# Optimization experiments

Measured on AMD Instinct MI355X. Metric: run time of the kernel, lower is better.

## Reference

```python
import jax, jax.numpy as jnp
import numpy as np

D_MODEL = 1024
N_HEADS = 16
HEAD_DIM = D_MODEL // N_HEADS  # 64


def setup_inputs() -> dict:
    key = jax.random.key(0)
    ks = jax.random.split(key, 6)
    scale_in = 1.0 / np.sqrt(D_MODEL)
    scale_hd = 1.0 / np.sqrt(N_HEADS * HEAD_DIM)
    inputs_q = jax.random.normal(ks[0], (4, 2048, D_MODEL), dtype=jnp.float32)
    # DenseGeneral kernels: [d_model, n_heads, head_dim] for q/k/v, [n_heads, head_dim, d_model] for out.
    Wq = jax.random.normal(ks[1], (D_MODEL, N_HEADS, HEAD_DIM), dtype=jnp.float32) * scale_in
    Wk = jax.random.normal(ks[2], (D_MODEL, N_HEADS, HEAD_DIM), dtype=jnp.float32) * scale_in
    Wv = jax.random.normal(ks[3], (D_MODEL, N_HEADS, HEAD_DIM), dtype=jnp.float32) * scale_in
    Wo = jax.random.normal(ks[4], (N_HEADS, HEAD_DIM, D_MODEL), dtype=jnp.float32) * scale_hd
    bq = jnp.zeros((N_HEADS, HEAD_DIM), dtype=jnp.float32)
    bk = jnp.zeros((N_HEADS, HEAD_DIM), dtype=jnp.float32)
    bv = jnp.zeros((N_HEADS, HEAD_DIM), dtype=jnp.float32)
    bo = jnp.zeros((D_MODEL,), dtype=jnp.float32)
    return {"inputs_q": inputs_q, "Wq": Wq, "bq": bq, "Wk": Wk, "bk": bk,
            "Wv": Wv, "bv": bv, "Wo": Wo, "bo": bo}


def reference(inputs_q, Wq, bq, Wk, bk, Wv, bv, Wo, bo):
    # Self-attention: inputs_kv = inputs_q.
    # QKV projections (DenseGeneral axis=-1 -> (heads, head_dim)).
    q = jnp.einsum('bsf,fhd->bshd', inputs_q, Wq) + bq  # [B,S,H,D]
    k = jnp.einsum('bsf,fhd->bshd', inputs_q, Wk) + bk
    v = jnp.einsum('bsf,fhd->bshd', inputs_q, Wv) + bv
    # Scaled dot-product attention (naive: full [B,H,S,S] scores, as in source).
    q = q / jnp.sqrt(jnp.asarray(HEAD_DIM, dtype=q.dtype))
    scores = jnp.einsum('bqhd,bkhd->bhqk', q, k)  # [B,H,Sq,Sk]
    attn = jax.nn.softmax(scores, axis=-1)
    x = jnp.einsum('bhqk,bkhd->bqhd', attn, v)  # [B,S,H,D]
    # Output projection over (heads, head_dim).
    out = jnp.einsum('bqhd,hdf->bqf', x, Wo) + bo  # [B,S,d_model]
    return out
```

## Files before the change

kernel.cpp:

```cpp
#include <hip/hip_runtime.h>
#include <math.h>

typedef __bf16 bf16;
typedef __attribute__((ext_vector_type(4))) __bf16 bf16x4;
typedef __attribute__((ext_vector_type(8))) __bf16 bf16x8;
typedef __attribute__((ext_vector_type(4))) float f32x4;

#define LOG2E 1.44269504088896340736f

__device__ __forceinline__ f32x4 mfma16(bf16x8 a, bf16x8 b, f32x4 c) {
  return __builtin_amdgcn_mfma_f32_16x16x32_bf16(a, b, c, 0, 0, 0);
}

__device__ __forceinline__ void load_lds16(const bf16* g, bf16* l) {
  __builtin_amdgcn_global_load_lds(
      (__attribute__((address_space(1))) void*)(g),
      (__attribute__((address_space(3))) void*)(l), 16, 0, 0);
}

__global__ __launch_bounds__(256) void cvt_x(const float* __restrict__ x,
                                             bf16* __restrict__ xb) {
  int i = (blockIdx.x * 256 + threadIdx.x) * 8;
  float4 a = *(const float4*)&x[i];
  float4 b = *(const float4*)&x[i + 4];
  bf16x8 v;
  v[0] = (bf16)a.x; v[1] = (bf16)a.y; v[2] = (bf16)a.z; v[3] = (bf16)a.w;
  v[4] = (bf16)b.x; v[5] = (bf16)b.y; v[6] = (bf16)b.z; v[7] = (bf16)b.w;
  *(bf16x8*)&xb[i] = v;
}

__global__ __launch_bounds__(256) void wtrans(
    const float* __restrict__ Wq, const float* __restrict__ Wk,
    const float* __restrict__ Wv, const float* __restrict__ Wo,
    bf16* __restrict__ Wcat, bf16* __restrict__ WoT, float qscale) {
  __shared__ float t[32][33];
  const int z = blockIdx.z;
  const float* src = (z == 0) ? Wq : (z == 1) ? Wk : (z == 2) ? Wv : Wo;
  bf16* dst = (z == 3) ? WoT : (Wcat + (size_t)z * 1024 * 1024);
  const float scale = (z == 0) ? qscale : 1.0f;
  int c0 = blockIdx.x * 32, r0 = blockIdx.y * 32;
  for (int i = threadIdx.y; i < 32; i += 8)
    t[i][threadIdx.x] = src[(r0 + i) * 1024 + c0 + threadIdx.x];
  __syncthreads();
  for (int i = threadIdx.y; i < 32; i += 8)
    dst[(c0 + i) * 1024 + r0 + threadIdx.x] = (bf16)(t[threadIdx.x][i] * scale);
}

__global__ __launch_bounds__(256) void vtrans(const bf16* __restrict__ Vs,
                                              bf16* __restrict__ Vt) {
  __shared__ bf16 t[64][72];
  const int bh = blockIdx.y;
  const int s0 = blockIdx.x * 64;
  const size_t base = (size_t)bh * 2048 * 64;
  const int tid = threadIdx.x;
  {
    int r = tid >> 3, c = (tid & 7) * 8;
    *(uint4*)&t[r][c]      = *(const uint4*)&Vs[base + (size_t)(s0 + r) * 64 + c];
    *(uint4*)&t[r + 32][c] = *(const uint4*)&Vs[base + (size_t)(s0 + r + 32) * 64 + c];
  }
  __syncthreads();
  int d = tid >> 2, sc = (tid & 3) * 16;
  bf16 tmp[16];
#pragma unroll
  for (int k = 0; k < 16; k++) tmp[k] = t[sc + k][d];
  *(uint4*)&Vt[base + (size_t)d * 2048 + s0 + sc]     = *(uint4*)&tmp[0];
  *(uint4*)&Vt[base + (size_t)d * 2048 + s0 + sc + 8] = *(uint4*)&tmp[8];
}

template <int MODE>
__global__ __launch_bounds__(256, 2) void gemm_bt(
    const bf16* __restrict__ A, const bf16* __restrict__ Bt, int N, int K,
    bf16* __restrict__ Qo, bf16* __restrict__ Ko, bf16* __restrict__ Vo,
    const float* __restrict__ b0, const float* __restrict__ b1,
    const float* __restrict__ b2,
    float* __restrict__ Co, const float* __restrict__ bias) {
  __shared__ bf16 lA[128 * 32];
  __shared__ bf16 lB[128 * 32];
  const int tid = threadIdx.x;
  const int lane = tid & 63, w = tid >> 6;
  const int l16 = lane & 15, quad = lane >> 4;
  const int swz = (l16 >> 2) & 3;
  const int wm = w >> 1, wn = w & 1;
  const int id = blockIdx.x;
  const int xcd = id & 7, local = id >> 3;
  const int m0 = (xcd * 8 + (local & 7)) * 128;
  const int n0 = (local >> 3) * 128;

  const int srow = w * 16 + (lane >> 2);
  const int scol = (((lane & 3) ^ ((lane >> 4) & 3)) * 8);
  const bf16* Ag = A + (size_t)(m0 + srow) * K + scol;
  const bf16* Bg = Bt + (size_t)(n0 + srow) * K + scol;
  bf16* lAw = &lA[w * 16 * 32];
  bf16* lBw = &lB[w * 16 * 32];

  f32x4 acc[4][4] = {};
  for (int k0 = 0; k0 < K; k0 += 32) {
    __syncthreads();
    load_lds16(Ag + k0, lAw);
    load_lds16(Ag + k0 + (size_t)64 * K, lAw + 64 * 32);
    load_lds16(Bg + k0, lBw);
    load_lds16(Bg + k0 + (size_t)64 * K, lBw + 64 * 32);
    __syncthreads();
    bf16x8 af[4], bfr[4];
#pragma unroll
    for (int i = 0; i < 4; i++)
      af[i] = *(const bf16x8*)&lA[(wm * 64 + i * 16 + l16) * 32 + (quad ^ swz) * 8];
#pragma unroll
    for (int i = 0; i < 4; i++)
      bfr[i] = *(const bf16x8*)&lB[(wn * 64 + i * 16 + l16) * 32 + (quad ^ swz) * 8];
#pragma unroll
    for (int i = 0; i < 4; i++)
#pragma unroll
      for (int j = 0; j < 4; j++)
        acc[i][j] = mfma16(af[i], bfr[j], acc[i][j]);
  }

  if (MODE == 0) {
    const int which = n0 >> 10;
    bf16* dst = (which == 0) ? Qo : (which == 1) ? Ko : Vo;
    const float* bsrc = (which == 0) ? b0 : (which == 1) ? b1 : b2;
    const float bscale = (which == 0) ? (0.125f * LOG2E) : 1.0f;
#pragma unroll
    for (int j = 0; j < 4; j++) {
      const int nn = (n0 & 1023) + wn * 64 + j * 16 + l16;
      const int h = nn >> 6, d = nn & 63;
      const float bias_v = bsrc[nn] * bscale;
#pragma unroll
      for (int i = 0; i < 4; i++) {
#pragma unroll
        for (int rg = 0; rg < 4; rg++) {
          const int grow = m0 + wm * 64 + i * 16 + quad * 4 + rg;
          const int bb = grow >> 11, s = grow & 2047;
          dst[((size_t)(bb * 16 + h) * 2048 + s) * 64 + d] =
              (bf16)(acc[i][j][rg] + bias_v);
        }
      }
    }
  } else {
#pragma unroll
    for (int j = 0; j < 4; j++) {
      const int gcol = n0 + wn * 64 + j * 16 + l16;
      const float bias_v = bias[gcol];
#pragma unroll
      for (int i = 0; i < 4; i++) {
#pragma unroll
        for (int rg = 0; rg < 4; rg++) {
          const int grow = m0 + wm * 64 + i * 16 + quad * 4 + rg;
          Co[(size_t)grow * N + gcol] = acc[i][j][rg] + bias_v;
        }
      }
    }
  }
}

__global__ __launch_bounds__(256, 2) void attn(const bf16* __restrict__ Q,
                                               const bf16* __restrict__ Kb,
                                               const bf16* __restrict__ Vt,
                                               bf16* __restrict__ X2) {
  __shared__ bf16 lK[2][2][64][32];
  __shared__ bf16 lV[2][2][64][32];
  __shared__ bf16 lP[4][64][72];
  const int tid = threadIdx.x;
  const int lane = tid & 63, w = tid >> 6;
  const int l16 = lane & 15, quad = lane >> 4;
  const int swz = (l16 >> 2) & 3;
  const int bh = blockIdx.x & 63;
  const int q0 = (blockIdx.x >> 6) * 256;
  const int bb = bh >> 4, h = bh & 15;
  const size_t base = (size_t)bh * 2048 * 64;

  bf16x8 aq[4][2];
#pragma unroll
  for (int mi = 0; mi < 4; mi++)
#pragma unroll
    for (int kh = 0; kh < 2; kh++)
      aq[mi][kh] = *(const bf16x8*)&Q[base + (size_t)(q0 + w * 64 + mi * 16 + l16) * 64 + kh * 32 + quad * 8];

  f32x4 o_acc[4][4] = {};
  float l_r[4] = {0.f, 0.f, 0.f, 0.f};

  const int drow = lane >> 2;
  const int dcol = (((lane & 3) ^ ((lane >> 4) & 3)) * 8);
  const bf16* Kg = Kb + base + (size_t)(w * 16 + drow) * 64 + dcol;
  const bf16* Vg = Vt + base + (size_t)(w * 16 + drow) * 2048 + dcol;

  load_lds16(Kg, &lK[0][0][w * 16][0]);
  load_lds16(Kg + 32, &lK[0][1][w * 16][0]);
  load_lds16(Vg, &lV[0][0][w * 16][0]);
  load_lds16(Vg + 32, &lV[0][1][w * 16][0]);

  for (int kt = 0; kt < 32; kt++) {
    const int p = kt & 1;
    __syncthreads();
    if (kt + 1 < 32) {
      const bf16* kg = Kg + (size_t)(kt + 1) * 64 * 64;
      const bf16* vg = Vg + (kt + 1) * 64;
      load_lds16(kg, &lK[p ^ 1][0][w * 16][0]);
      load_lds16(kg + 32, &lK[p ^ 1][1][w * 16][0]);
      load_lds16(vg, &lV[p ^ 1][0][w * 16][0]);
      load_lds16(vg + 32, &lV[p ^ 1][1][w * 16][0]);
    }

#pragma unroll
    for (int g = 0; g < 2; g++) {
      f32x4 s[2][4] = {};
#pragma unroll
      for (int n2 = 0; n2 < 2; n2++) {
        const int ni = g * 2 + n2;
        bf16x8 ak0 = *(const bf16x8*)&lK[p][0][ni * 16 + l16][(quad ^ swz) * 8];
        bf16x8 ak1 = *(const bf16x8*)&lK[p][1][ni * 16 + l16][(quad ^ swz) * 8];
#pragma unroll
        for (int mi = 0; mi < 4; mi++) {
          s[n2][mi] = mfma16(ak0, aq[mi][0], s[n2][mi]);
          s[n2][mi] = mfma16(ak1, aq[mi][1], s[n2][mi]);
        }
      }
#pragma unroll
      for (int n2 = 0; n2 < 2; n2++) {
        const int ni = g * 2 + n2;
#pragma unroll
        for (int mi = 0; mi < 4; mi++) {
          bf16x4 pw;
          float lp = 0.f;
#pragma unroll
          for (int rg = 0; rg < 4; rg++) {
            float pv = __builtin_amdgcn_exp2f(s[n2][mi][rg]);
            lp += pv;
            pw[rg] = (bf16)pv;
          }
          l_r[mi] += lp;
          *(bf16x4*)&lP[w][mi * 16 + l16][ni * 16 + quad * 4] = pw;
        }
      }
    }

    bf16x8 vf0[4], vf1[4];
#pragma unroll
    for (int di = 0; di < 4; di++) {
      vf0[di] = *(const bf16x8*)&lV[p][0][di * 16 + l16][(quad ^ swz) * 8];
      vf1[di] = *(const bf16x8*)&lV[p][1][di * 16 + l16][(quad ^ swz) * 8];
    }
#pragma unroll
    for (int mi = 0; mi < 4; mi++) {
      bf16x8 ap0 = *(const bf16x8*)&lP[w][mi * 16 + l16][quad * 8];
      bf16x8 ap1 = *(const bf16x8*)&lP[w][mi * 16 + l16][32 + quad * 8];
#pragma unroll
      for (int di = 0; di < 4; di++) {
        o_acc[mi][di] = mfma16(ap0, vf0[di], o_acc[mi][di]);
        o_acc[mi][di] = mfma16(ap1, vf1[di], o_acc[mi][di]);
      }
    }
  }

#pragma unroll
  for (int mi = 0; mi < 4; mi++) {
    float l = l_r[mi];
    l += __shfl_xor(l, 16);
    l += __shfl_xor(l, 32);
    l_r[mi] = 1.f / l;
  }
#pragma unroll
  for (int mi = 0; mi < 4; mi++)
#pragma unroll
    for (int rg = 0; rg < 4; rg++) {
      float inv = __shfl(l_r[mi], quad * 4 + rg);
      int s = q0 + w * 64 + mi * 16 + quad * 4 + rg;
#pragma unroll
      for (int di = 0; di < 4; di++) {
        float v = o_acc[mi][di][rg] * inv;
        X2[((size_t)bb * 2048 + s) * 1024 + h * 64 + di * 16 + l16] = (bf16)v;
      }
    }
}

extern "C" void kernel_launch(void* const* d_in, const int* in_sizes, int n_in,
                              void* d_out, int out_size, void* d_ws, size_t ws_size,
                              hipStream_t stream) {
  const float* x  = (const float*)d_in[0];
  const float* Wq = (const float*)d_in[1];
  const float* bq = (const float*)d_in[2];
  const float* Wk = (const float*)d_in[3];
  const float* bk = (const float*)d_in[4];
  const float* Wv = (const float*)d_in[5];
  const float* bv = (const float*)d_in[6];
  const float* Wo = (const float*)d_in[7];
  const float* bo = (const float*)d_in[8];
  float* out = (float*)d_out;

  char* ws = (char*)d_ws;
  bf16* Xb   = (bf16*)(ws);
  bf16* Wcat = (bf16*)(ws + 16777216);
  bf16* WoT  = (bf16*)(ws + 23068672);
  bf16* Qb   = (bf16*)(ws + 25165824);
  bf16* Kbf  = (bf16*)(ws + 41943040);
  bf16* Vt   = (bf16*)(ws + 58720256);
  bf16* Vs   = (bf16*)d_out;
  bf16* X2   = Xb;

  cvt_x<<<4096, 256, 0, stream>>>(x, Xb);
  wtrans<<<dim3(32, 32, 4), dim3(32, 8), 0, stream>>>(
      Wq, Wk, Wv, Wo, Wcat, WoT, 0.125f * LOG2E);

  gemm_bt<0><<<1536, 256, 0, stream>>>(Xb, Wcat, 3072, 1024,
      Qb, Kbf, Vs, bq, bk, bv, nullptr, nullptr);

  vtrans<<<dim3(32, 64), 256, 0, stream>>>(Vs, Vt);

  attn<<<512, 256, 0, stream>>>(Qb, Kbf, Vt, X2);

  gemm_bt<1><<<512, 256, 0, stream>>>(X2, WoT, 1024, 1024,
      nullptr, nullptr, nullptr, nullptr, nullptr, nullptr, out, bo);
}
```

Before: 276.2 us.

## Load K/V fragments directly from global memory in single-wave attention blocks

The attention kernel switches from 256-thread blocks that stage K and V tiles in double-buffered shared memory to 64-thread single-wave blocks that read K and V MFMA fragments straight from global memory, leaving only the P tile in LDS. This removes the block-wide barriers and LDS staging traffic and raises the number of blocks from 512 to 2048. In exchange each wave now fetches K/V itself without reuse across waves, so global/L2 traffic grows fourfold, and nothing prefetches ahead of use, so load latency has to be covered by occupancy instead.

```diff
diff --git a/kernel.cpp b/kernel.cpp
--- a/kernel.cpp
+++ b/kernel.cpp
@@ -153,19 +153,15 @@
   }
 }
 
-__global__ __launch_bounds__(256, 2) void attn(const bf16* __restrict__ Q,
-                                               const bf16* __restrict__ Kb,
-                                               const bf16* __restrict__ Vt,
-                                               bf16* __restrict__ X2) {
-  __shared__ bf16 lK[2][2][64][32];
-  __shared__ bf16 lV[2][2][64][32];
-  __shared__ bf16 lP[4][64][72];
-  const int tid = threadIdx.x;
-  const int lane = tid & 63, w = tid >> 6;
+__global__ __launch_bounds__(64, 3) void attn(const bf16* __restrict__ Q,
+                                              const bf16* __restrict__ Kb,
+                                              const bf16* __restrict__ Vt,
+                                              bf16* __restrict__ X2) {
+  __shared__ bf16 lP[64][72];
+  const int lane = threadIdx.x;
   const int l16 = lane & 15, quad = lane >> 4;
-  const int swz = (l16 >> 2) & 3;
   const int bh = blockIdx.x & 63;
-  const int q0 = (blockIdx.x >> 6) * 256;
+  const int q0 = (blockIdx.x >> 6) * 64;
   const int bb = bh >> 4, h = bh & 15;
   const size_t base = (size_t)bh * 2048 * 64;
 
@@ -174,41 +170,24 @@
   for (int mi = 0; mi < 4; mi++)
 #pragma unroll
     for (int kh = 0; kh < 2; kh++)
-      aq[mi][kh] = *(const bf16x8*)&Q[base + (size_t)(q0 + w * 64 + mi * 16 + l16) * 64 + kh * 32 + quad * 8];
+      aq[mi][kh] = *(const bf16x8*)&Q[base + (size_t)(q0 + mi * 16 + l16) * 64 + kh * 32 + quad * 8];
 
   f32x4 o_acc[4][4] = {};
   float l_r[4] = {0.f, 0.f, 0.f, 0.f};
 
-  const int drow = lane >> 2;
-  const int dcol = (((lane & 3) ^ ((lane >> 4) & 3)) * 8);
-  const bf16* Kg = Kb + base + (size_t)(w * 16 + drow) * 64 + dcol;
-  const bf16* Vg = Vt + base + (size_t)(w * 16 + drow) * 2048 + dcol;
-
-  load_lds16(Kg, &lK[0][0][w * 16][0]);
-  load_lds16(Kg + 32, &lK[0][1][w * 16][0]);
-  load_lds16(Vg, &lV[0][0][w * 16][0]);
-  load_lds16(Vg + 32, &lV[0][1][w * 16][0]);
+  const bf16* Kp = Kb + base + (size_t)l16 * 64 + quad * 8;
+  const bf16* Vp = Vt + base + (size_t)l16 * 2048 + quad * 8;
 
   for (int kt = 0; kt < 32; kt++) {
-    const int p = kt & 1;
-    __syncthreads();
-    if (kt + 1 < 32) {
-      const bf16* kg = Kg + (size_t)(kt + 1) * 64 * 64;
-      const bf16* vg = Vg + (kt + 1) * 64;
-      load_lds16(kg, &lK[p ^ 1][0][w * 16][0]);
-      load_lds16(kg + 32, &lK[p ^ 1][1][w * 16][0]);
-      load_lds16(vg, &lV[p ^ 1][0][w * 16][0]);
-      load_lds16(vg + 32, &lV[p ^ 1][1][w * 16][0]);
-    }
-
 #pragma unroll
     for (int g = 0; g < 2; g++) {
       f32x4 s[2][4] = {};
 #pragma unroll
       for (int n2 = 0; n2 < 2; n2++) {
         const int ni = g * 2 + n2;
-        bf16x8 ak0 = *(const bf16x8*)&lK[p][0][ni * 16 + l16][(quad ^ swz) * 8];
-        bf16x8 ak1 = *(const bf16x8*)&lK[p][1][ni * 16 + l16][(quad ^ swz) * 8];
+        const bf16* kr = Kp + (size_t)(kt * 64 + ni * 16) * 64;
+        bf16x8 ak0 = *(const bf16x8*)kr;
+        bf16x8 ak1 = *(const bf16x8*)(kr + 32);
 #pragma unroll
         for (int mi = 0; mi < 4; mi++) {
           s[n2][mi] = mfma16(ak0, aq[mi][0], s[n2][mi]);
@@ -229,7 +208,7 @@
             pw[rg] = (bf16)pv;
           }
           l_r[mi] += lp;
-          *(bf16x4*)&lP[w][mi * 16 + l16][ni * 16 + quad * 4] = pw;
+          *(bf16x4*)&lP[mi * 16 + l16][ni * 16 + quad * 4] = pw;
         }
       }
     }
@@ -237,13 +216,14 @@
     bf16x8 vf0[4], vf1[4];
 #pragma unroll
     for (int di = 0; di < 4; di++) {
-      vf0[di] = *(const bf16x8*)&lV[p][0][di * 16 + l16][(quad ^ swz) * 8];
-      vf1[di] = *(const bf16x8*)&lV[p][1][di * 16 + l16][(quad ^ swz) * 8];
+      const bf16* vr = Vp + (size_t)(di * 16) * 2048 + kt * 64;
+      vf0[di] = *(const bf16x8*)vr;
+      vf1[di] = *(const bf16x8*)(vr + 32);
     }
 #pragma unroll
     for (int mi = 0; mi < 4; mi++) {
-      bf16x8 ap0 = *(const bf16x8*)&lP[w][mi * 16 + l16][quad * 8];
-      bf16x8 ap1 = *(const bf16x8*)&lP[w][mi * 16 + l16][32 + quad * 8];
+      bf16x8 ap0 = *(const bf16x8*)&lP[mi * 16 + l16][quad * 8];
+      bf16x8 ap1 = *(const bf16x8*)&lP[mi * 16 + l16][32 + quad * 8];
 #pragma unroll
       for (int di = 0; di < 4; di++) {
         o_acc[mi][di] = mfma16(ap0, vf0[di], o_acc[mi][di]);
@@ -264,7 +244,7 @@
 #pragma unroll
     for (int rg = 0; rg < 4; rg++) {
       float inv = __shfl(l_r[mi], quad * 4 + rg);
-      int s = q0 + w * 64 + mi * 16 + quad * 4 + rg;
+      int s = q0 + mi * 16 + quad * 4 + rg;
 #pragma unroll
       for (int di = 0; di < 4; di++) {
         float v = o_acc[mi][di][rg] * inv;
@@ -306,7 +286,7 @@
 
   vtrans<<<dim3(32, 64), 256, 0, stream>>>(Vs, Vt);
 
-  attn<<<512, 256, 0, stream>>>(Qb, Kbf, Vt, X2);
+  attn<<<2048, 64, 0, stream>>>(Qb, Kbf, Vt, X2);
 
   gemm_bt<1><<<512, 256, 0, stream>>>(X2, WoT, 1024, 1024,
       nullptr, nullptr, nullptr, nullptr, nullptr, nullptr, out, bo);
```

After: 334.0 us. 1.21x slower.

## Fuse V transpose into QKV GEMM epilogue and merge prep kernels

Applied to the files above, without the earlier changes.

Removes the separate vtrans kernel by having the QKV GEMM write V directly in transposed [b,h,d,s] layout. For V tiles it swaps the A/B operand roles so each lane's accumulator runs along the sequence dimension, which keeps the transposed stores contiguous. It also merges the input conversion and weight transpose kernels into a single launch. The intent is to cut launch overhead and the extra read/write pass over V, at the cost of more branching inside the GEMM.

```diff
diff --git a/kernel.cpp b/kernel.cpp
--- a/kernel.cpp
+++ b/kernel.cpp
@@ -18,53 +18,35 @@
       (__attribute__((address_space(3))) void*)(l), 16, 0, 0);
 }
 
-__global__ __launch_bounds__(256) void cvt_x(const float* __restrict__ x,
-                                             bf16* __restrict__ xb) {
-  int i = (blockIdx.x * 256 + threadIdx.x) * 8;
-  float4 a = *(const float4*)&x[i];
-  float4 b = *(const float4*)&x[i + 4];
-  bf16x8 v;
-  v[0] = (bf16)a.x; v[1] = (bf16)a.y; v[2] = (bf16)a.z; v[3] = (bf16)a.w;
-  v[4] = (bf16)b.x; v[5] = (bf16)b.y; v[6] = (bf16)b.z; v[7] = (bf16)b.w;
-  *(bf16x8*)&xb[i] = v;
-}
-
-__global__ __launch_bounds__(256) void wtrans(
-    const float* __restrict__ Wq, const float* __restrict__ Wk,
-    const float* __restrict__ Wv, const float* __restrict__ Wo,
+__global__ __launch_bounds__(256) void prep(
+    const float* __restrict__ x, const float* __restrict__ Wq,
+    const float* __restrict__ Wk, const float* __restrict__ Wv,
+    const float* __restrict__ Wo, bf16* __restrict__ Xb,
     bf16* __restrict__ Wcat, bf16* __restrict__ WoT, float qscale) {
-  __shared__ float t[32][33];
-  const int z = blockIdx.z;
-  const float* src = (z == 0) ? Wq : (z == 1) ? Wk : (z == 2) ? Wv : Wo;
-  bf16* dst = (z == 3) ? WoT : (Wcat + (size_t)z * 1024 * 1024);
-  const float scale = (z == 0) ? qscale : 1.0f;
-  int c0 = blockIdx.x * 32, r0 = blockIdx.y * 32;
-  for (int i = threadIdx.y; i < 32; i += 8)
-    t[i][threadIdx.x] = src[(r0 + i) * 1024 + c0 + threadIdx.x];
-  __syncthreads();
-  for (int i = threadIdx.y; i < 32; i += 8)
-    dst[(c0 + i) * 1024 + r0 + threadIdx.x] = (bf16)(t[threadIdx.x][i] * scale);
-}
-
-__global__ __launch_bounds__(256) void vtrans(const bf16* __restrict__ Vs,
-                                              bf16* __restrict__ Vt) {
-  __shared__ bf16 t[64][72];
-  const int bh = blockIdx.y;
-  const int s0 = blockIdx.x * 64;
-  const size_t base = (size_t)bh * 2048 * 64;
-  const int tid = threadIdx.x;
-  {
-    int r = tid >> 3, c = (tid & 7) * 8;
-    *(uint4*)&t[r][c]      = *(const uint4*)&Vs[base + (size_t)(s0 + r) * 64 + c];
-    *(uint4*)&t[r + 32][c] = *(const uint4*)&Vs[base + (size_t)(s0 + r + 32) * 64 + c];
-  }
-  __syncthreads();
-  int d = tid >> 2, sc = (tid & 3) * 16;
-  bf16 tmp[16];
-#pragma unroll
-  for (int k = 0; k < 16; k++) tmp[k] = t[sc + k][d];
-  *(uint4*)&Vt[base + (size_t)d * 2048 + s0 + sc]     = *(uint4*)&tmp[0];
-  *(uint4*)&Vt[base + (size_t)d * 2048 + s0 + sc + 8] = *(uint4*)&tmp[8];
+  const int id = blockIdx.x, tid = threadIdx.x;
+  if (id < 4096) {
+    int i = (id * 256 + tid) * 8;
+    float4 a = *(const float4*)&x[i];
+    float4 b = *(const float4*)&x[i + 4];
+    bf16x8 v;
+    v[0] = (bf16)a.x; v[1] = (bf16)a.y; v[2] = (bf16)a.z; v[3] = (bf16)a.w;
+    v[4] = (bf16)b.x; v[5] = (bf16)b.y; v[6] = (bf16)b.z; v[7] = (bf16)b.w;
+    *(bf16x8*)&Xb[i] = v;
+  } else {
+    __shared__ float t[32][33];
+    const int id2 = id - 4096;
+    const int z = id2 >> 10, tile = id2 & 1023;
+    const float* src = (z == 0) ? Wq : (z == 1) ? Wk : (z == 2) ? Wv : Wo;
+    bf16* dst = (z == 3) ? WoT : (Wcat + (size_t)z * 1024 * 1024);
+    const float scale = (z == 0) ? qscale : 1.0f;
+    const int c0 = (tile & 31) * 32, r0 = (tile >> 5) * 32;
+    const int tx = tid & 31, ty = tid >> 5;
+    for (int i = ty; i < 32; i += 8)
+      t[i][tx] = src[(r0 + i) * 1024 + c0 + tx];
+    __syncthreads();
+    for (int i = ty; i < 32; i += 8)
+      dst[(c0 + i) * 1024 + r0 + tx] = (bf16)(t[tx][i] * scale);
+  }
 }
 
 template <int MODE>
@@ -93,6 +75,12 @@
   bf16* lAw = &lA[w * 16 * 32];
   bf16* lBw = &lB[w * 16 * 32];
 
+  const bool vsw = (MODE == 0) && ((n0 >> 10) == 2);
+  const bf16* aSrc = vsw ? lB : lA;
+  const bf16* bSrc = vsw ? lA : lB;
+  const int aOff = vsw ? wn * 64 : wm * 64;
+  const int bOff = vsw ? wm * 64 : wn * 64;
+
   f32x4 acc[4][4] = {};
   for (int k0 = 0; k0 < K; k0 += 32) {
     __syncthreads();
@@ -104,10 +92,10 @@
     bf16x8 af[4], bfr[4];
 #pragma unroll
     for (int i = 0; i < 4; i++)
-      af[i] = *(const bf16x8*)&lA[(wm * 64 + i * 16 + l16) * 32 + (quad ^ swz) * 8];
+      af[i] = *(const bf16x8*)&aSrc[(aOff + i * 16 + l16) * 32 + (quad ^ swz) * 8];
 #pragma unroll
     for (int i = 0; i < 4; i++)
-      bfr[i] = *(const bf16x8*)&lB[(wn * 64 + i * 16 + l16) * 32 + (quad ^ swz) * 8];
+      bfr[i] = *(const bf16x8*)&bSrc[(bOff + i * 16 + l16) * 32 + (quad ^ swz) * 8];
 #pragma unroll
     for (int i = 0; i < 4; i++)
 #pragma unroll
@@ -117,22 +105,40 @@
 
   if (MODE == 0) {
     const int which = n0 >> 10;
-    bf16* dst = (which == 0) ? Qo : (which == 1) ? Ko : Vo;
-    const float* bsrc = (which == 0) ? b0 : (which == 1) ? b1 : b2;
-    const float bscale = (which == 0) ? (0.125f * LOG2E) : 1.0f;
-#pragma unroll
-    for (int j = 0; j < 4; j++) {
-      const int nn = (n0 & 1023) + wn * 64 + j * 16 + l16;
-      const int h = nn >> 6, d = nn & 63;
-      const float bias_v = bsrc[nn] * bscale;
+    if (which == 2) {
+      const int nnb = (n0 & 1023) + wn * 64;
+      const int bb = m0 >> 11, sbase = (m0 & 2047) + wm * 64;
 #pragma unroll
       for (int i = 0; i < 4; i++) {
 #pragma unroll
         for (int rg = 0; rg < 4; rg++) {
-          const int grow = m0 + wm * 64 + i * 16 + quad * 4 + rg;
-          const int bb = grow >> 11, s = grow & 2047;
-          dst[((size_t)(bb * 16 + h) * 2048 + s) * 64 + d] =
-              (bf16)(acc[i][j][rg] + bias_v);
+          const int nn = nnb + i * 16 + quad * 4 + rg;
+          const int h = nn >> 6, d = nn & 63;
+          const float bias_v = b2[nn];
+          bf16* dst = Vo + ((size_t)(bb * 16 + h) * 64 + d) * 2048 + sbase;
+#pragma unroll
+          for (int j = 0; j < 4; j++)
+            dst[j * 16 + l16] = (bf16)(acc[i][j][rg] + bias_v);
+        }
+      }
+    } else {
+      bf16* dst = (which == 0) ? Qo : Ko;
+      const float* bsrc = (which == 0) ? b0 : b1;
+      const float bscale = (which == 0) ? (0.125f * LOG2E) : 1.0f;
+#pragma unroll
+      for (int j = 0; j < 4; j++) {
+        const int nn = (n0 & 1023) + wn * 64 + j * 16 + l16;
+        const int h = nn >> 6, d = nn & 63;
+        const float bias_v = bsrc[nn] * bscale;
+#pragma unroll
+        for (int i = 0; i < 4; i++) {
+#pragma unroll
+          for (int rg = 0; rg < 4; rg++) {
+            const int grow = m0 + wm * 64 + i * 16 + quad * 4 + rg;
+            const int bb = grow >> 11, s = grow & 2047;
+            dst[((size_t)(bb * 16 + h) * 2048 + s) * 64 + d] =
+                (bf16)(acc[i][j][rg] + bias_v);
+          }
         }
       }
     }
@@ -294,17 +300,13 @@
   bf16* Qb   = (bf16*)(ws + 25165824);
   bf16* Kbf  = (bf16*)(ws + 41943040);
   bf16* Vt   = (bf16*)(ws + 58720256);
-  bf16* Vs   = (bf16*)d_out;
   bf16* X2   = Xb;
 
-  cvt_x<<<4096, 256, 0, stream>>>(x, Xb);
-  wtrans<<<dim3(32, 32, 4), dim3(32, 8), 0, stream>>>(
-      Wq, Wk, Wv, Wo, Wcat, WoT, 0.125f * LOG2E);
+  prep<<<8192, 256, 0, stream>>>(x, Wq, Wk, Wv, Wo, Xb, Wcat, WoT,
+                                 0.125f * LOG2E);
 
   gemm_bt<0><<<1536, 256, 0, stream>>>(Xb, Wcat, 3072, 1024,
-      Qb, Kbf, Vs, bq, bk, bv, nullptr, nullptr);
-
-  vtrans<<<dim3(32, 64), 256, 0, stream>>>(Vs, Vt);
+      Qb, Kbf, Vt, bq, bk, bv, nullptr, nullptr);
 
   attn<<<512, 256, 0, stream>>>(Qb, Kbf, Vt, X2);
 
```

Result: no change. 279.9 us (+1.4%).
